# Kernel tuning notes

Measured on AMD Instinct MI355X. Metric: run time of the kernel, lower is better.

The kernel has to match this reference:

```python
import jax, jax.numpy as jnp
import numpy as np

D_MODEL = 1024
NUM_HEADS = 16
D_K = D_MODEL // NUM_HEADS
B, S = 2, 2048


def setup_inputs() -> dict:
    key = jax.random.key(0)
    ks = jax.random.split(key, 6)
    scale = 1.0 / np.sqrt(D_MODEL)
    x = jax.random.normal(ks[0], (B, S, D_MODEL), dtype=jnp.float32)
    # causal mask: 1 where masked (future positions), per masked_fill(mask == 1, -inf)
    mask = jnp.triu(jnp.ones((S, S), dtype=jnp.int32), k=1)
    Wq = jax.random.normal(ks[1], (D_MODEL, D_MODEL), dtype=jnp.float32) * scale
    Wk = jax.random.normal(ks[2], (D_MODEL, D_MODEL), dtype=jnp.float32) * scale
    Wv = jax.random.normal(ks[3], (D_MODEL, D_MODEL), dtype=jnp.float32) * scale
    Wo = jax.random.normal(ks[4], (D_MODEL, D_MODEL), dtype=jnp.float32) * scale
    zeros = jnp.zeros((D_MODEL,), dtype=jnp.float32)
    return {"x": x, "mask": mask, "Wq": Wq, "bq": zeros, "Wk": Wk, "bk": zeros,
            "Wv": Wv, "bv": zeros, "Wo": Wo, "bo": zeros}


def reference(x, mask, Wq, bq, Wk, bk, Wv, bv, Wo, bo):
    b, s, d = x.shape
    # linear projections (torch nn.Linear: x @ W^T + b; here W stored as [in, out])
    Q = x @ Wq + bq
    K = x @ Wk + bk
    V = x @ Wv + bv
    # split heads -> (b, h, s, d_k)
    def split(t):
        return t.reshape(b, s, NUM_HEADS, D_K).transpose(0, 2, 1, 3)
    Q, K, V = split(Q), split(K), split(V)
    scale = 1.0 / jnp.sqrt(jnp.float32(D_K))
    scores = jnp.einsum("bhqd,bhkd->bhqk", Q, K) * scale  # (b,h,s,s)
    scores = jnp.where(mask[None, None, :, :] == 1, -jnp.inf, scores)
    attn = jax.nn.softmax(scores, axis=-1)
    out = jnp.einsum("bhqk,bhkd->bhqd", attn, V)
    out = out.transpose(0, 2, 1, 3).reshape(b, s, d)  # concat heads
    return out @ Wo + bo
```

## Files before the change

kernel.cpp:

```cpp
#include <hip/hip_runtime.h>
#include <hip/hip_bf16.h>
#include <cstdint>
#include <cmath>

#define DM 1024
#define NH 16
#define DK 64
#define NB 2
#define SS 2048
#define MM (NB*SS)

typedef unsigned short u16;
typedef uint32_t u32;
typedef __attribute__((ext_vector_type(4))) float f32x4;
typedef __attribute__((ext_vector_type(8))) short s16x8;
typedef __attribute__((ext_vector_type(2))) uint32_t u32x2;

__device__ __forceinline__ u16 f2bf(float f) {
    __hip_bfloat16 h = __float2bfloat16(f);
    return __builtin_bit_cast(u16, h);
}
__device__ __forceinline__ float bf2f(u16 u) {
    u32 x = (u32)u << 16;
    return __builtin_bit_cast(float, x);
}

__device__ __forceinline__ u32 cvtpk(float a, float b) {
    u32 r;
    asm("v_cvt_pk_bf16_f32 %0, %1, %2" : "=v"(r) : "v"(a), "v"(b));
    return r;
}

__device__ __forceinline__ void gload_lds16(void* lds, const void* g) {
    __builtin_amdgcn_global_load_lds(
        (const __attribute__((address_space(1))) uint32_t*)g,
        (__attribute__((address_space(3))) uint32_t*)lds, 16, 0, 0);
}

__device__ __forceinline__ int swz(int row, int cb) {
    return row * 128 + ((((cb) >> 4) ^ (row & 7)) << 4) + ((cb) & 15);
}

#define FENCE_BAR  do { __builtin_amdgcn_sched_barrier(0); \
                        __builtin_amdgcn_s_barrier();      \
                        __builtin_amdgcn_sched_barrier(0); } while (0)

__global__ void mha_prep(const float* __restrict__ x, u16* __restrict__ xb,
                         const float* __restrict__ W0, const float* __restrict__ W1,
                         const float* __restrict__ W2, const float* __restrict__ W3,
                         u16* __restrict__ WtBase) {
    const int bid = blockIdx.x, tid = threadIdx.x;
    if (bid < 4096) {
        int i = (bid * 256 + tid) * 4;
        float4 v = *reinterpret_cast<const float4*>(x + i);
        ushort4 o;
        o.x = f2bf(v.x); o.y = f2bf(v.y); o.z = f2bf(v.z); o.w = f2bf(v.w);
        *reinterpret_cast<ushort4*>(xb + i) = o;
        return;
    }
    __shared__ float t[32][33];
    const int b2 = bid - 4096;
    const int mat = b2 >> 10, rem = b2 & 1023;
    const int cx = rem & 31, cy = rem >> 5;
    const float* W = (mat == 0) ? W0 : (mat == 1) ? W1 : (mat == 2) ? W2 : W3;
    u16* Wt = WtBase + (size_t)mat * DM * DM;
    const int c0 = cx * 32, r0 = cy * 32;
    const int tx = tid & 31, ty = tid >> 5;
#pragma unroll
    for (int i = ty; i < 32; i += 8)
        t[i][tx] = W[(size_t)(r0 + i) * DM + c0 + tx];
    __syncthreads();
#pragma unroll
    for (int i = ty; i < 32; i += 8)
        Wt[(size_t)(c0 + i) * DM + r0 + tx] = f2bf(t[tx][i]);
}

__device__ __forceinline__ void gemm_loop(const u16* __restrict__ A, const u16* __restrict__ Bt,
                                          int m0, int n0,
                                          u16 (*As)[64], u16 (*Bs)[64], f32x4 acc[4][4]) {
    const int tid = threadIdx.x;
    const int wave = tid >> 6, lane = tid & 63;
    const int lr = lane & 15, kg = lane >> 4;
    const int wr = wave >> 1, wc = wave & 1;

    for (int k0 = 0; k0 < DM; k0 += 64) {
        __syncthreads();
#pragma unroll
        for (int i = 0; i < 4; ++i) {
            const int o   = ((wave * 4 + i) * 64 + lane) * 16;
            const int row = o >> 7;
            const int kb  = o & 127;
            gload_lds16((char*)As + o, A  + (size_t)(m0 + row) * DM + k0 + (kb >> 1));
            gload_lds16((char*)Bs + o, Bt + (size_t)(n0 + row) * DM + k0 + (kb >> 1));
        }
        __syncthreads();
#pragma unroll
        for (int kk = 0; kk < 64; kk += 32) {
            s16x8 a[4], b[4];
#pragma unroll
            for (int m = 0; m < 4; ++m)
                a[m] = *reinterpret_cast<const s16x8*>(&As[wr * 64 + m * 16 + lr][kk + kg * 8]);
#pragma unroll
            for (int n = 0; n < 4; ++n)
                b[n] = *reinterpret_cast<const s16x8*>(&Bs[wc * 64 + n * 16 + lr][kk + kg * 8]);
#pragma unroll
            for (int m = 0; m < 4; ++m)
#pragma unroll
                for (int n = 0; n < 4; ++n)
                    acc[m][n] = __builtin_amdgcn_mfma_f32_16x16x32_bf16(a[m], b[n], acc[m][n], 0, 0, 0);
        }
    }
}

__global__ __launch_bounds__(256, 2) void mha_gemm_qkv(const u16* __restrict__ xb, const u16* __restrict__ Wt,
                                                       const float* __restrict__ bq, const float* __restrict__ bk,
                                                       const float* __restrict__ bv, u16* __restrict__ qkv) {
    __shared__ __align__(16) char smem[32768];
    u16 (*As)[64] = reinterpret_cast<u16(*)[64]>(smem);
    u16 (*Bs)[64] = reinterpret_cast<u16(*)[64]>(smem + 16384);

    const int bid = blockIdx.x;
    const int j = bid & 7, r = bid >> 3;
    const int bx = j * 4 + (r & 3);
    const int by = (r >> 2) & 7;
    const int z  = r >> 5;
    const int m0 = bx * 128, n0 = by * 128;

    const float* bias = (z == 0) ? bq : (z == 1) ? bk : bv;
    const float scale = (z == 0) ? 0.125f * 1.44269504088896f : 1.0f;
    u16* Cout = qkv + (size_t)z * MM * DM;

    f32x4 acc[4][4] = {};
    gemm_loop(xb, Wt + (size_t)z * DM * DM, m0, n0, As, Bs, acc);

    const int tid = threadIdx.x;
    const int wave = tid >> 6, lane = tid & 63;
    const int lr = lane & 15, kg = lane >> 4;
    const int wr = wave >> 1, wc = wave & 1;

    __syncthreads();
#pragma unroll
    for (int m = 0; m < 4; ++m)
#pragma unroll
        for (int n = 0; n < 4; ++n) {
            const int col = wc * 64 + n * 16 + lr;
            const float bv2 = bias[n0 + col];
#pragma unroll
            for (int j2 = 0; j2 < 4; ++j2) {
                const int row = wr * 64 + m * 16 + kg * 4 + j2;
                const float v = (acc[m][n][j2] + bv2) * scale;
                int imgoff;
                if (z == 0) {
                    imgoff = row * 256 + (col >> 6) * 128 + (col & 63) * 2;
                } else if (z == 1) {
                    imgoff = ((row >> 6) * 2 + (col >> 6)) * 8192 + swz(row & 63, (col & 63) * 2);
                } else {
                    imgoff = ((row >> 6) * 2 + (col >> 6)) * 8192
                           + swz(col & 63, ((row & 63) >> 1) * 4 + (row & 1) * 2);
                }
                *reinterpret_cast<u16*>(smem + imgoff) = f2bf(v);
            }
        }
    __syncthreads();
    const int bb = m0 >> 11, s0 = m0 & (SS - 1);
    const int kt0 = s0 >> 6, h0 = n0 >> 6;
#pragma unroll
    for (int it = 0; it < 8; ++it) {
        const int c = it * 256 + tid;
        const s16x8 v = *reinterpret_cast<const s16x8*>(smem + c * 16);
        u16* dst;
        if (z == 0) {
            const int srow = c >> 4, inrow = c & 15;
            const int hl = inrow >> 3, d0 = (inrow & 7) * 8;
            dst = Cout + (((size_t)(bb * NH + h0 + hl) * SS + (s0 + srow)) * DK) + d0;
        } else {
            const int quad = c >> 9, off = (c & 511) * 8;
            const int ktl = quad >> 1, hl = quad & 1;
            dst = Cout + ((size_t)(bb * NH + h0 + hl) * 32 + kt0 + ktl) * 4096 + off;
        }
        *reinterpret_cast<s16x8*>(dst) = v;
    }
}

__device__ __forceinline__ void gemm_loop_db(const u16* __restrict__ A, const u16* __restrict__ Bt,
                                             int m0, int n0, char* smem , f32x4 acc[4][4]) {
    const int tid = threadIdx.x;
    const int wave = tid >> 6, lane = tid & 63;
    const int lr = lane & 15, kg = lane >> 4;
    const int wr = wave >> 1, wc = wave & 1;

    auto STAGE = [&](int buf, int k0) {
        char* As = smem + buf * 32768;
        char* Bs = As + 16384;
#pragma unroll
        for (int i = 0; i < 4; ++i) {
            const int o   = ((wave * 4 + i) * 64 + lane) * 16;
            const int row = o >> 7;
            const int kb  = o & 127;
            gload_lds16(As + o, A  + (size_t)(m0 + row) * DM + k0 + (kb >> 1));
            gload_lds16(Bs + o, Bt + (size_t)(n0 + row) * DM + k0 + (kb >> 1));
        }
    };

    STAGE(0, 0);
    for (int t = 0; t < 16; ++t) {
        if (t + 1 < 16) {
            STAGE((t + 1) & 1, (t + 1) * 64);
            asm volatile("s_waitcnt vmcnt(8)" ::: "memory");
        } else {
            asm volatile("s_waitcnt vmcnt(0)" ::: "memory");
        }
        FENCE_BAR;
        const u16 (*As)[64] = reinterpret_cast<const u16(*)[64]>(smem + (t & 1) * 32768);
        const u16 (*Bs)[64] = reinterpret_cast<const u16(*)[64]>(smem + (t & 1) * 32768 + 16384);
#pragma unroll
        for (int kk = 0; kk < 64; kk += 32) {
            s16x8 a[4], b[4];
#pragma unroll
            for (int m = 0; m < 4; ++m)
                a[m] = *reinterpret_cast<const s16x8*>(&As[wr * 64 + m * 16 + lr][kk + kg * 8]);
#pragma unroll
            for (int n = 0; n < 4; ++n)
                b[n] = *reinterpret_cast<const s16x8*>(&Bs[wc * 64 + n * 16 + lr][kk + kg * 8]);
#pragma unroll
            for (int m = 0; m < 4; ++m)
#pragma unroll
                for (int n = 0; n < 4; ++n)
                    acc[m][n] = __builtin_amdgcn_mfma_f32_16x16x32_bf16(a[m], b[n], acc[m][n], 0, 0, 0);
        }
        FENCE_BAR;
    }
}

__global__ __launch_bounds__(256, 2) void mha_gemm_out(const u16* __restrict__ AO, const u16* __restrict__ WoT,
                                                       const float* __restrict__ bo, float* __restrict__ out) {
    __shared__ __align__(16) char smem[65536];
    const int m0 = blockIdx.x * 128, n0 = blockIdx.y * 128;

    f32x4 acc[4][4] = {};
    gemm_loop_db(AO, WoT, m0, n0, smem, acc);

    const int tid = threadIdx.x;
    const int wave = tid >> 6, lane = tid & 63;
    const int lr = lane & 15, kg = lane >> 4;
    const int wr = wave >> 1, wc = wave & 1;
#pragma unroll
    for (int m = 0; m < 4; ++m)
#pragma unroll
        for (int n = 0; n < 4; ++n) {
            const int col = n0 + wc * 64 + n * 16 + lr;
            const float bv = bo[col];
#pragma unroll
            for (int j2 = 0; j2 < 4; ++j2) {
                const int row = m0 + wr * 64 + m * 16 + kg * 4 + j2;
                out[(size_t)row * DM + col] = acc[m][n][j2] + bv;
            }
        }
}

__device__ const unsigned char JQT[24] = {
    7,15,15, 14,14, 6,13,13, 12,12, 5,11,11, 10,10, 4,9,9, 8,8, 3,2,1,0};
__device__ const unsigned char JKS[24] = {
    0,0,16, 0,15, 0,0,14, 0,13, 0,0,12, 0,11, 0,0,10, 0,9, 0,0,0,0};
__device__ const unsigned char JKL[24] = {
    16,16,16, 15,15, 14,14,14, 13,13, 12,12,12, 11,11, 10,10,10, 9,9, 8,6,4,2};
__device__ const unsigned char JSL[24] = {
    255,14,15, 12,13, 255,10,11, 8,9, 255,6,7, 4,5, 255,2,3, 0,1, 255,255,255,255};

__global__ __launch_bounds__(512, 4) void mha_attn(const u16* __restrict__ Qb, const u16* __restrict__ Kswz,
                                                   const u16* __restrict__ Vtswz, u16* __restrict__ AO,
                                                   u16* __restrict__ Opart, float* __restrict__ lpart) {
    __shared__ __align__(16) char lds[49152];

    const int bid = blockIdx.x;
    const int bh  = bid & 31;
    const int job = bid >> 5;
    const int qt   = JQT[job];
    const int kst  = JKS[job];
    const int klen = JKL[job];
    const int slot = JSL[job];
    const int qb = qt * 128;

    const int tid = threadIdx.x, w = tid >> 6, lane = tid & 63;
    const int lr = lane & 15, kg = lane >> 4;

    const u16* Qh = Qb + (size_t)bh * SS * DK;
    const char* Ktiles = (const char*)(Kswz  + (size_t)bh * 32 * 4096);
    const char* Vtiles = (const char*)(Vtswz + (size_t)bh * 32 * 4096);
    const int bb = bh >> 4, hh = bh & (NH - 1);
    char* psb = lds + 32768 + w * 2048;
    const int o = tid * 16;

    const int qrow = qb + w * 16 + lr;
    const s16x8 qf0 = *reinterpret_cast<const s16x8*>(Qh + (size_t)qrow * DK + kg * 8);
    const s16x8 qf1 = *reinterpret_cast<const s16x8*>(Qh + (size_t)qrow * DK + 32 + kg * 8);
    f32x4 accO[4] = {};
    float lp = 0.f;

    const int kend = kst + klen;
    gload_lds16(lds + o,         Ktiles + kst * 8192 + o);
    gload_lds16(lds + 16384 + o, Vtiles + kst * 8192 + o);

    for (int t = kst; t < kend; ++t) {
        const int buf = (t - kst) & 1;
        asm volatile("s_waitcnt vmcnt(0)" ::: "memory");
        __syncthreads();
        if (t + 1 < kend) {
            gload_lds16(lds + (buf ^ 1) * 8192 + o,         Ktiles + (t + 1) * 8192 + o);
            gload_lds16(lds + 16384 + (buf ^ 1) * 8192 + o, Vtiles + (t + 1) * 8192 + o);
        }
        const char* ksb = lds + buf * 8192;
        const char* vtb = lds + 16384 + buf * 8192;
        const int kb = t * 64;

        f32x4 sc[4];
#pragma unroll
        for (int f = 0; f < 4; ++f) {
            s16x8 kf0 = *reinterpret_cast<const s16x8*>(ksb + swz(f * 16 + lr, kg * 16));
            s16x8 kf1 = *reinterpret_cast<const s16x8*>(ksb + swz(f * 16 + lr, 64 + kg * 16));
            f32x4 s = {};
            s = __builtin_amdgcn_mfma_f32_16x16x32_bf16(kf0, qf0, s, 0, 0, 0);
            s = __builtin_amdgcn_mfma_f32_16x16x32_bf16(kf1, qf1, s, 0, 0, 0);
            sc[f] = s;
        }
#pragma unroll
        for (int f = 0; f < 4; ++f)
#pragma unroll
            for (int j = 0; j < 4; ++j)
                sc[f][j] = __builtin_amdgcn_exp2f(sc[f][j]);
        if (kb + 63 > qb + w * 16) {
            const int qg = qb + w * 16 + lr;
#pragma unroll
            for (int f = 0; f < 4; ++f) {
                const int kc = kb + f * 16 + kg * 4;
#pragma unroll
                for (int j = 0; j < 4; ++j)
                    if (kc + j > qg) sc[f][j] = 0.f;
            }
        }
        float fs0 = 0.f, fs1 = 0.f;
#pragma unroll
        for (int f = 0; f < 4; ++f) {
            u32x2 pp;
            pp[0] = cvtpk(sc[f][0], sc[f][1]);
            pp[1] = cvtpk(sc[f][2], sc[f][3]);
            *reinterpret_cast<u32x2*>(psb + swz(lr, f * 32 + kg * 8)) = pp;
            const float s01 = sc[f][0] + sc[f][1], s23 = sc[f][2] + sc[f][3];
            if (f & 1) fs1 += s01 + s23; else fs0 += s01 + s23;
        }
        lp += fs0 + fs1;

        const s16x8 pf0 = *reinterpret_cast<const s16x8*>(psb + swz(lr, kg * 16));
        const s16x8 pf1 = *reinterpret_cast<const s16x8*>(psb + swz(lr, 64 + kg * 16));
#pragma unroll
        for (int db = 0; db < 4; ++db) {
            s16x8 vf0 = *reinterpret_cast<const s16x8*>(vtb + swz(db * 16 + lr, kg * 16));
            s16x8 vf1 = *reinterpret_cast<const s16x8*>(vtb + swz(db * 16 + lr, 64 + kg * 16));
            accO[db] = __builtin_amdgcn_mfma_f32_16x16x32_bf16(pf0, vf0, accO[db], 0, 0, 0);
            accO[db] = __builtin_amdgcn_mfma_f32_16x16x32_bf16(pf1, vf1, accO[db], 0, 0, 0);
        }
    }

    lp += __shfl_xor(lp, 16, 64);
    lp += __shfl_xor(lp, 32, 64);

    if (slot == 255) {
        float inv[4];
#pragma unroll
        for (int j = 0; j < 4; ++j)
            inv[j] = 1.0f / __shfl(lp, kg * 4 + j, 64);
#pragma unroll
        for (int db = 0; db < 4; ++db) {
            const int d = db * 16 + lr;
#pragma unroll
            for (int j = 0; j < 4; ++j) {
                const int s = qb + w * 16 + kg * 4 + j;
                AO[((size_t)(bb * SS + s)) * DM + hh * DK + d] = f2bf(accO[db][j] * inv[j]);
            }
        }
    } else {
        const int idx = bh * 16 + slot;
        u16* Od = Opart + (size_t)idx * 8192;
#pragma unroll
        for (int db = 0; db < 4; ++db) {
            const int d = db * 16 + lr;
#pragma unroll
            for (int j = 0; j < 4; ++j)
                Od[(w * 16 + kg * 4 + j) * 64 + d] = f2bf(accO[db][j]);
        }
        if (lane < 16)
            lpart[idx * 128 + w * 16 + lane] = lp;
    }
}

__global__ __launch_bounds__(256) void mha_combine(const u16* __restrict__ Opart,
                                                   const float* __restrict__ lpart,
                                                   u16* __restrict__ AO) {
    const int blk = blockIdx.x;
    const int bh = blk & 31, q = blk >> 5;
    const int qt = 8 + q;
    const int t = threadIdx.x;
    const int row = t >> 1, c0 = (t & 1) * 32;
    const int idx0 = bh * 16 + q * 2;
    const u16* O0 = Opart + (size_t)idx0 * 8192 + row * 64 + c0;
    const u16* O1 = O0 + 8192;
    const float l = lpart[idx0 * 128 + row] + lpart[(idx0 + 1) * 128 + row];
    const float inv = 1.0f / l;
    const int bb = bh >> 4, hh = bh & (NH - 1);
    const int s = qt * 128 + row;
    u16* dst = AO + ((size_t)(bb * SS + s)) * DM + hh * DK + c0;
#pragma unroll
    for (int h = 0; h < 4; ++h) {
        s16x8 a = *reinterpret_cast<const s16x8*>(O0 + h * 8);
        s16x8 b = *reinterpret_cast<const s16x8*>(O1 + h * 8);
        u16* ap = (u16*)&a; u16* bp = (u16*)&b;
        u16 ov[8];
#pragma unroll
        for (int i = 0; i < 8; ++i)
            ov[i] = f2bf((bf2f(ap[i]) + bf2f(bp[i])) * inv);
        *reinterpret_cast<ushort4*>(dst + h * 8) = *reinterpret_cast<ushort4*>(&ov[0]);
        *reinterpret_cast<ushort4*>(dst + h * 8 + 4) = *reinterpret_cast<ushort4*>(&ov[4]);
    }
}

extern "C" void kernel_launch(void* const* d_in, const int* in_sizes, int n_in,
                              void* d_out, int out_size, void* d_ws, size_t ws_size,
                              hipStream_t stream) {
    const float* x  = (const float*)d_in[0];
    const float* Wq = (const float*)d_in[2];
    const float* bq = (const float*)d_in[3];
    const float* Wk = (const float*)d_in[4];
    const float* bk = (const float*)d_in[5];
    const float* Wv = (const float*)d_in[6];
    const float* bv = (const float*)d_in[7];
    const float* Wo = (const float*)d_in[8];
    const float* bo = (const float*)d_in[9];
    float* out = (float*)d_out;

    char* ws = (char*)d_ws;
    u16* xb  = (u16*)(ws);
    u16* Wt  = (u16*)(ws + ((size_t)8  << 20));
    u16* qkv = (u16*)(ws + ((size_t)16 << 20));
    u16* AO  = (u16*)(ws + ((size_t)40 << 20));
    u16*   Opart = (u16*)(ws);
    float* lpart = (float*)(ws + ((size_t)8 << 20));

    mha_prep<<<dim3(8192), dim3(256), 0, stream>>>(x, xb, Wq, Wk, Wv, Wo, Wt);
    mha_gemm_qkv<<<dim3(768), dim3(256), 0, stream>>>(xb, Wt, bq, bk, bv, qkv);
    mha_attn<<<dim3(768), dim3(512), 0, stream>>>(qkv, qkv + (size_t)4194304, qkv + (size_t)8388608,
                                                  AO, Opart, lpart);
    mha_combine<<<dim3(256), dim3(256), 0, stream>>>(Opart, lpart, AO);
    mha_gemm_out<<<dim3(32, 8), dim3(256), 0, stream>>>(AO, Wt + (size_t)3 * DM * DM, bo, out);
}
```

Before: 102.7 us.

## Rework QKV GEMM with 128x192 tiles, double-buffered swizzled LDS staging

Rewrites the fused QKV projection GEMM to use 128x192 output tiles spanning Q/K/V columns (512 blocks instead of 768), with double-buffered async global-to-LDS loads and an XOR-swizzled LDS layout to avoid bank conflicts. The epilogue no longer stages through LDS for coalesced 16-byte stores; each lane writes scattered 2-byte values directly into the head-split and tiled K/V layouts. The aim is more reuse per block, overlap of loads with MFMA, and fewer LDS conflicts. The cost is 80KB of LDS, which limits occupancy, and uncoalesced output stores.

```diff
diff --git a/kernel.cpp b/kernel.cpp
--- a/kernel.cpp
+++ b/kernel.cpp
@@ -75,111 +75,93 @@
         Wt[(size_t)(c0 + i) * DM + r0 + tx] = f2bf(t[tx][i]);
 }
 
-__device__ __forceinline__ void gemm_loop(const u16* __restrict__ A, const u16* __restrict__ Bt,
-                                          int m0, int n0,
-                                          u16 (*As)[64], u16 (*Bs)[64], f32x4 acc[4][4]) {
+__global__ __launch_bounds__(256, 2) void mha_gemm_qkv(const u16* __restrict__ xb, const u16* __restrict__ Wt,
+                                                       const float* __restrict__ bq, const float* __restrict__ bk,
+                                                       const float* __restrict__ bv, u16* __restrict__ qkv) {
+    __shared__ __align__(16) char smem[81920];
+
+    const int bid = blockIdx.x;
+    const int bx = bid & 31, by = bid >> 5;
+    const int m0 = bx * 128, n0g = by * 192;
+
     const int tid = threadIdx.x;
     const int wave = tid >> 6, lane = tid & 63;
     const int lr = lane & 15, kg = lane >> 4;
     const int wr = wave >> 1, wc = wave & 1;
 
-    for (int k0 = 0; k0 < DM; k0 += 64) {
-        __syncthreads();
+    auto STAGE = [&](int buf, int kt) {
 #pragma unroll
         for (int i = 0; i < 4; ++i) {
-            const int o   = ((wave * 4 + i) * 64 + lane) * 16;
-            const int row = o >> 7;
-            const int kb  = o & 127;
-            gload_lds16((char*)As + o, A  + (size_t)(m0 + row) * DM + k0 + (kb >> 1));
-            gload_lds16((char*)Bs + o, Bt + (size_t)(n0 + row) * DM + k0 + (kb >> 1));
-        }
-        __syncthreads();
-#pragma unroll
-        for (int kk = 0; kk < 64; kk += 32) {
-            s16x8 a[4], b[4];
+            const int o = tid * 16 + i * 4096;
+            const int r = o >> 7, slot = (o >> 4) & 7;
+            gload_lds16(smem + buf * 16384 + o,
+                        xb + (size_t)(m0 + r) * DM + kt * 64 + ((slot ^ (r & 7)) << 3));
+        }
+#pragma unroll
+        for (int i = 0; i < 6; ++i) {
+            const int o = tid * 16 + i * 4096;
+            const int r = o >> 7, slot = (o >> 4) & 7;
+            gload_lds16(smem + 32768 + buf * 24576 + o,
+                        Wt + (size_t)(n0g + r) * DM + kt * 64 + ((slot ^ (r & 7)) << 3));
+        }
+    };
+
+    f32x4 acc[4][6] = {};
+    STAGE(0, 0);
+    for (int t = 0; t < 16; ++t) {
+        if (t + 1 < 16) {
+            STAGE((t + 1) & 1, t + 1);
+            asm volatile("s_waitcnt vmcnt(10)" ::: "memory");
+        } else {
+            asm volatile("s_waitcnt vmcnt(0)" ::: "memory");
+        }
+        FENCE_BAR;
+        const char* Ab = smem + (t & 1) * 16384;
+        const char* Bb = smem + 32768 + (t & 1) * 24576;
+#pragma unroll
+        for (int ks = 0; ks < 2; ++ks) {
+            s16x8 a[4], b[6];
 #pragma unroll
             for (int m = 0; m < 4; ++m)
-                a[m] = *reinterpret_cast<const s16x8*>(&As[wr * 64 + m * 16 + lr][kk + kg * 8]);
-#pragma unroll
-            for (int n = 0; n < 4; ++n)
-                b[n] = *reinterpret_cast<const s16x8*>(&Bs[wc * 64 + n * 16 + lr][kk + kg * 8]);
+                a[m] = *reinterpret_cast<const s16x8*>(Ab + swz(wr * 64 + m * 16 + lr, ks * 64 + kg * 16));
+#pragma unroll
+            for (int n = 0; n < 6; ++n)
+                b[n] = *reinterpret_cast<const s16x8*>(Bb + swz(wc * 96 + n * 16 + lr, ks * 64 + kg * 16));
 #pragma unroll
             for (int m = 0; m < 4; ++m)
 #pragma unroll
-                for (int n = 0; n < 4; ++n)
+                for (int n = 0; n < 6; ++n)
                     acc[m][n] = __builtin_amdgcn_mfma_f32_16x16x32_bf16(a[m], b[n], acc[m][n], 0, 0, 0);
         }
-    }
-}
-
-__global__ __launch_bounds__(256, 2) void mha_gemm_qkv(const u16* __restrict__ xb, const u16* __restrict__ Wt,
-                                                       const float* __restrict__ bq, const float* __restrict__ bk,
-                                                       const float* __restrict__ bv, u16* __restrict__ qkv) {
-    __shared__ __align__(16) char smem[32768];
-    u16 (*As)[64] = reinterpret_cast<u16(*)[64]>(smem);
-    u16 (*Bs)[64] = reinterpret_cast<u16(*)[64]>(smem + 16384);
-
-    const int bid = blockIdx.x;
-    const int j = bid & 7, r = bid >> 3;
-    const int bx = j * 4 + (r & 3);
-    const int by = (r >> 2) & 7;
-    const int z  = r >> 5;
-    const int m0 = bx * 128, n0 = by * 128;
-
-    const float* bias = (z == 0) ? bq : (z == 1) ? bk : bv;
-    const float scale = (z == 0) ? 0.125f * 1.44269504088896f : 1.0f;
-    u16* Cout = qkv + (size_t)z * MM * DM;
-
-    f32x4 acc[4][4] = {};
-    gemm_loop(xb, Wt + (size_t)z * DM * DM, m0, n0, As, Bs, acc);
-
-    const int tid = threadIdx.x;
-    const int wave = tid >> 6, lane = tid & 63;
-    const int lr = lane & 15, kg = lane >> 4;
-    const int wr = wave >> 1, wc = wave & 1;
-
-    __syncthreads();
+        FENCE_BAR;
+    }
+
 #pragma unroll
     for (int m = 0; m < 4; ++m)
 #pragma unroll
-        for (int n = 0; n < 4; ++n) {
-            const int col = wc * 64 + n * 16 + lr;
-            const float bv2 = bias[n0 + col];
-#pragma unroll
-            for (int j2 = 0; j2 < 4; ++j2) {
-                const int row = wr * 64 + m * 16 + kg * 4 + j2;
-                const float v = (acc[m][n][j2] + bv2) * scale;
-                int imgoff;
+        for (int n = 0; n < 6; ++n) {
+            const int colg = n0g + wc * 96 + n * 16 + lr;
+            const int z = colg >> 10, coll = colg & 1023;
+            const int h = coll >> 6, d = coll & 63;
+            const float bv2 = ((z == 0) ? bq : (z == 1) ? bk : bv)[coll];
+            const float scale = (z == 0) ? 0.125f * 1.44269504088896f : 1.0f;
+            u16* Cout = qkv + (size_t)z * MM * DM;
+#pragma unroll
+            for (int j = 0; j < 4; ++j) {
+                const int row = m0 + wr * 64 + m * 16 + kg * 4 + j;
+                const int bb = row >> 11, s = row & (SS - 1);
+                const float v = (acc[m][n][j] + bv2) * scale;
                 if (z == 0) {
-                    imgoff = row * 256 + (col >> 6) * 128 + (col & 63) * 2;
-                } else if (z == 1) {
-                    imgoff = ((row >> 6) * 2 + (col >> 6)) * 8192 + swz(row & 63, (col & 63) * 2);
+                    Cout[(((size_t)(bb * NH + h) * SS + s) * DK) + d] = f2bf(v);
                 } else {
-                    imgoff = ((row >> 6) * 2 + (col >> 6)) * 8192
-                           + swz(col & 63, ((row & 63) >> 1) * 4 + (row & 1) * 2);
+                    const int kt = s >> 6, r = s & 63;
+                    const size_t tb = ((size_t)(bb * NH + h) * 32 + kt) * 4096;
+                    const int bo = (z == 1) ? swz(r, d * 2)
+                                            : swz(d, (r >> 1) * 4 + (r & 1) * 2);
+                    Cout[tb + (bo >> 1)] = f2bf(v);
                 }
-                *reinterpret_cast<u16*>(smem + imgoff) = f2bf(v);
             }
         }
-    __syncthreads();
-    const int bb = m0 >> 11, s0 = m0 & (SS - 1);
-    const int kt0 = s0 >> 6, h0 = n0 >> 6;
-#pragma unroll
-    for (int it = 0; it < 8; ++it) {
-        const int c = it * 256 + tid;
-        const s16x8 v = *reinterpret_cast<const s16x8*>(smem + c * 16);
-        u16* dst;
-        if (z == 0) {
-            const int srow = c >> 4, inrow = c & 15;
-            const int hl = inrow >> 3, d0 = (inrow & 7) * 8;
-            dst = Cout + (((size_t)(bb * NH + h0 + hl) * SS + (s0 + srow)) * DK) + d0;
-        } else {
-            const int quad = c >> 9, off = (c & 511) * 8;
-            const int ktl = quad >> 1, hl = quad & 1;
-            dst = Cout + ((size_t)(bb * NH + h0 + hl) * 32 + kt0 + ktl) * 4096 + off;
-        }
-        *reinterpret_cast<s16x8*>(dst) = v;
-    }
 }
 
 __device__ __forceinline__ void gemm_loop_db(const u16* __restrict__ A, const u16* __restrict__ Bt,
@@ -446,7 +428,7 @@
     float* lpart = (float*)(ws + ((size_t)8 << 20));
 
     mha_prep<<<dim3(8192), dim3(256), 0, stream>>>(x, xb, Wq, Wk, Wv, Wo, Wt);
-    mha_gemm_qkv<<<dim3(768), dim3(256), 0, stream>>>(xb, Wt, bq, bk, bv, qkv);
+    mha_gemm_qkv<<<dim3(512), dim3(256), 0, stream>>>(xb, Wt, bq, bk, bv, qkv);
     mha_attn<<<dim3(768), dim3(512), 0, stream>>>(qkv, qkv + (size_t)4194304, qkv + (size_t)8388608,
                                                   AO, Opart, lpart);
     mha_combine<<<dim3(256), dim3(256), 0, stream>>>(Opart, lpart, AO);
```

New measurement: 102.2 us. No clear change (-0.5%).
